# Kernel tuning notes

Measured on AMD Instinct MI355X. Metric: run time of the kernel, lower is better.

## Reference

```python
import jax, jax.numpy as jnp
import numpy as np

N_OBJECTS = 32  # mask labels 1..32 (0 = background)


def setup_inputs() -> dict:
    key = jax.random.key(0)
    k1, k2, k3, k4 = jax.random.split(key, 4)
    B, F, H, W = 8, 64, 256, 256
    encoded = jax.random.normal(k1, (B, F, H, W), dtype=jnp.float32)
    masks = jax.random.randint(k2, (B, 1, H, W), 0, N_OBJECTS + 1, dtype=jnp.int32)
    W1 = jax.random.normal(k3, (2 * F, F // 2), dtype=jnp.float32) * 0.05
    b1 = jnp.zeros((F // 2,), dtype=jnp.float32)
    W2 = jax.random.normal(k4, (F // 2, 4), dtype=jnp.float32) * 0.05
    b2 = jnp.zeros((4,), dtype=jnp.float32)
    return {"encoded": encoded, "masks": masks, "W1": W1, "b1": b1, "W2": W2, "b2": b2}


def reference(encoded, masks, W1, b1, W2, b2):
    B, F, H, W = encoded.shape
    # --- masked per-object max-pool (segment max over pixels) ---
    enc = encoded.reshape(B, F, H * W).transpose(0, 2, 1)  # [B, HW, F]
    ids = masks.reshape(B, H * W)                          # [B, HW]
    seg_max = jax.vmap(
        lambda d, i: jax.ops.segment_max(d, i, num_segments=N_OBJECTS + 1)
    )(enc, ids)                                            # [B, N+1, F]
    vectors = seg_max[:, 1:, :]                            # [B, N, F] (skip label 0)

    # --- O(N^2) pairwise MLP: connections[b,c,j,i] = sigmoid(MLP([v_i; v_j])) ---
    N = vectors.shape[1]
    vi = jnp.broadcast_to(vectors[:, :, None, :], (B, N, N, F))  # v_i over axis 1
    vj = jnp.broadcast_to(vectors[:, None, :, :], (B, N, N, F))  # v_j over axis 2
    pairs = jnp.concatenate([vi, vj], axis=-1)                   # [B, N, N, 2F]
    h = jnp.einsum('bijd,dh->bijh', pairs, W1) + b1
    out = jax.nn.sigmoid(jnp.einsum('bijh,hc->bijc', h, W2) + b2)  # [B, Ni, Nj, C]
    connections = out.transpose(0, 3, 2, 1)                        # [B, C, Nj, Ni]
    return vectors, connections
```

## Files before the change

kernel.cpp:

```cpp
#include <hip/hip_runtime.h>
#include <math.h>

#define B_      8
#define F_      64
#define HW_     65536
#define NSEG    33
#define NOBJ    32
#define FPB     8
#define SLICES  16
#define PIXB    (HW_ / SLICES)

__global__ __launch_bounds__(256) void segmax_kernel(
        const float* __restrict__ enc, const int* __restrict__ masks,
        float* __restrict__ part) {
    __shared__ float acc[FPB * NSEG * 32];
    const int tid = threadIdx.x;
    const int blk = blockIdx.x;
    const int b     = blk >> 7;
    const int fg    = (blk >> 4) & 7;
    const int slice = blk & 15;

    for (int i = tid; i < FPB * NSEG * 32; i += 256) acc[i] = -INFINITY;
    __syncthreads();

    const int fl = tid >> 5;
    const int l  = tid & 31;
    float* a = acc + fl * (NSEG * 32) + l;

    const float4* ep = (const float4*)(enc + ((size_t)(b * F_ + fg * FPB + fl)) * HW_
                                       + slice * PIXB) + l;
    const int4*   mp = (const int4*)(masks + (size_t)b * HW_ + slice * PIXB) + l;

    #pragma unroll 8
    for (int c = 0; c < PIXB / 128; ++c) {
        float4 v  = ep[c * 32];
        int4   id = mp[c * 32];
        float o;
        o = a[id.x * 32]; a[id.x * 32] = fmaxf(o, v.x);
        o = a[id.y * 32]; a[id.y * 32] = fmaxf(o, v.y);
        o = a[id.z * 32]; a[id.z * 32] = fmaxf(o, v.z);
        o = a[id.w * 32]; a[id.w * 32] = fmaxf(o, v.w);
    }
    __syncthreads();

    float* dst = part + ((size_t)(b * SLICES + slice) * NOBJ) * F_;
    {
        const int f = tid & 7, s = (tid >> 3) + 1;
        const float* row = acc + f * (NSEG * 32) + s * 32;
        float m = -INFINITY;
        #pragma unroll
        for (int k = 0; k < 32; k += 4) {
            float4 q = *(const float4*)(row + k);
            m = fmaxf(m, fmaxf(fmaxf(q.x, q.y), fmaxf(q.z, q.w)));
        }
        dst[(s - 1) * F_ + fg * FPB + f] = m;
    }
}

__global__ __launch_bounds__(256) void mlp_kernel(
        const float* __restrict__ part,
        const float* __restrict__ W1, const float* __restrict__ b1,
        const float* __restrict__ W2, const float* __restrict__ b2,
        float* __restrict__ out_vec, float* __restrict__ out_conn) {
    const int b   = blockIdx.x >> 2;
    const int it  = blockIdx.x & 3;
    const int tid = threadIdx.x;
    __shared__ float v[NOBJ * 68];
    __shared__ float w1s[2 * F_ * 32];
    __shared__ float w2s[32 * 4];
    __shared__ float b1s[32];
    __shared__ float Am[8 * 36];
    __shared__ float Bm[NOBJ * 36];

    for (int i = tid; i < 2 * F_ * 32 / 4; i += 256)
        ((float4*)w1s)[i] = ((const float4*)W1)[i];
    if (tid < 32) { w2s[tid*4+0]=W2[tid*4+0]; w2s[tid*4+1]=W2[tid*4+1];
                    w2s[tid*4+2]=W2[tid*4+2]; w2s[tid*4+3]=W2[tid*4+3];
                    b1s[tid] = b1[tid]; }

    const float4* p4 = (const float4*)(part + (size_t)b * SLICES * NOBJ * F_);
    for (int cell = tid; cell < NOBJ * 16; cell += 256) {
        const int s = cell >> 4, f4 = cell & 15;
        float4 m = {-INFINITY, -INFINITY, -INFINITY, -INFINITY};
        #pragma unroll
        for (int sl = 0; sl < SLICES; ++sl) {
            float4 q = p4[((size_t)sl * NOBJ + s) * (F_ / 4) + f4];
            m.x = fmaxf(m.x, q.x); m.y = fmaxf(m.y, q.y);
            m.z = fmaxf(m.z, q.z); m.w = fmaxf(m.w, q.w);
        }
        *(float4*)(v + s * 68 + f4 * 4) = m;
        if (it == 0) ((float4*)(out_vec + (size_t)b * NOBJ * F_))[cell] = m;
    }
    __syncthreads();

    for (int d = tid; d < 320; d += 256) {
        int kg, obj, half;
        if (d < 64) { half = 0; obj = it * 8 + (d >> 3); kg = d & 7; }
        else        { half = 1; obj = (d - 64) >> 3;     kg = d & 7; }
        const float* vv = v + obj * 68;
        const float* w  = w1s + half * (F_ * 32) + kg * 4;
        float4 s4 = {0.f, 0.f, 0.f, 0.f};
        #pragma unroll
        for (int f = 0; f < F_; ++f) {
            float4 wf = *(const float4*)(w + f * 32);
            float x = vv[f];
            s4.x = fmaf(x, wf.x, s4.x); s4.y = fmaf(x, wf.y, s4.y);
            s4.z = fmaf(x, wf.z, s4.z); s4.w = fmaf(x, wf.w, s4.w);
        }
        if (half == 0) {
            float4 bb = *(const float4*)(b1s + kg * 4);
            s4.x += bb.x; s4.y += bb.y; s4.z += bb.z; s4.w += bb.w;
            *(float4*)(Am + (d >> 3) * 36 + kg * 4) = s4;
        } else {
            *(float4*)(Bm + obj * 36 + kg * 4) = s4;
        }
    }
    __syncthreads();

    {
        int i_loc = tid >> 5, j = tid & 31;
        float o0 = b2[0], o1 = b2[1], o2 = b2[2], o3 = b2[3];
        #pragma unroll
        for (int kg = 0; kg < 8; ++kg) {
            float4 ha = *(const float4*)(Am + i_loc * 36 + kg * 4);
            float4 hb = *(const float4*)(Bm + j * 36 + kg * 4);
            float h0 = ha.x + hb.x, h1 = ha.y + hb.y;
            float h2 = ha.z + hb.z, h3 = ha.w + hb.w;
            const float* w2 = w2s + kg * 16;
            o0 = fmaf(h0, w2[0],  fmaf(h1, w2[4],  fmaf(h2, w2[8],  fmaf(h3, w2[12], o0))));
            o1 = fmaf(h0, w2[1],  fmaf(h1, w2[5],  fmaf(h2, w2[9],  fmaf(h3, w2[13], o1))));
            o2 = fmaf(h0, w2[2],  fmaf(h1, w2[6],  fmaf(h2, w2[10], fmaf(h3, w2[14], o2))));
            o3 = fmaf(h0, w2[3],  fmaf(h1, w2[7],  fmaf(h2, w2[11], fmaf(h3, w2[15], o3))));
        }
        float* oc = out_conn + (size_t)b * 4 * NOBJ * NOBJ + j * NOBJ + (it * 8 + i_loc);
        oc[0 * NOBJ * NOBJ] = 1.f / (1.f + expf(-o0));
        oc[1 * NOBJ * NOBJ] = 1.f / (1.f + expf(-o1));
        oc[2 * NOBJ * NOBJ] = 1.f / (1.f + expf(-o2));
        oc[3 * NOBJ * NOBJ] = 1.f / (1.f + expf(-o3));
    }
}

extern "C" void kernel_launch(void* const* d_in, const int* in_sizes, int n_in,
                              void* d_out, int out_size, void* d_ws, size_t ws_size,
                              hipStream_t stream) {
    const float* enc   = (const float*)d_in[0];
    const int*   masks = (const int*)  d_in[1];
    const float* W1    = (const float*)d_in[2];
    const float* b1    = (const float*)d_in[3];
    const float* W2    = (const float*)d_in[4];
    const float* b2    = (const float*)d_in[5];

    float* out_vec  = (float*)d_out;
    float* out_conn = out_vec + B_ * NOBJ * F_;
    float* part     = (float*)d_ws;

    segmax_kernel<<<B_ * (F_ / FPB) * SLICES, 256, 0, stream>>>(enc, masks, part);
    mlp_kernel<<<B_ * 4, 256, 0, stream>>>(part, W1, b1, W2, b2, out_vec, out_conn);
}
```

Measured before the change: 210.1 us.

## Fuse segment-max and pairwise MLP via last-block-done atomic counter

```diff
diff --git a/kernel.cpp b/kernel.cpp
--- a/kernel.cpp
+++ b/kernel.cpp
@@ -9,17 +9,35 @@
 #define FPB     8
 #define SLICES  16
 #define PIXB    (HW_ / SLICES)
+#define BLOCKS_PER_B ((F_ / FPB) * SLICES)
 
-__global__ __launch_bounds__(256) void segmax_kernel(
+union SharedU {
+    float acc[FPB * NSEG * 32];
+    struct {
+        float v[NOBJ * 68];
+        float w1s[2 * F_ * 32];
+        float w2s[NOBJ * 4];
+        float b1s[NOBJ];
+        float Cm[NOBJ * 36];
+        float Bm[NOBJ * 36];
+    } m;
+};
+
+__global__ __launch_bounds__(256) void fused_kernel(
         const float* __restrict__ enc, const int* __restrict__ masks,
-        float* __restrict__ part) {
-    __shared__ float acc[FPB * NSEG * 32];
+        const float* __restrict__ W1, const float* __restrict__ b1,
+        const float* __restrict__ W2, const float* __restrict__ b2,
+        float* __restrict__ part, int* __restrict__ cnt,
+        float* __restrict__ out_vec, float* __restrict__ out_conn) {
+    __shared__ SharedU sh;
+    __shared__ int is_last;
     const int tid = threadIdx.x;
     const int blk = blockIdx.x;
     const int b     = blk >> 7;
     const int fg    = (blk >> 4) & 7;
     const int slice = blk & 15;
 
+    float* acc = sh.acc;
     for (int i = tid; i < FPB * NSEG * 32; i += 256) acc[i] = -INFINITY;
     __syncthreads();
 
@@ -43,8 +61,8 @@
     }
     __syncthreads();
 
-    float* dst = part + ((size_t)(b * SLICES + slice) * NOBJ) * F_;
     {
+        float* dst = part + ((size_t)(b * SLICES + slice) * NOBJ) * F_;
         const int f = tid & 7, s = (tid >> 3) + 1;
         const float* row = acc + f * (NSEG * 32) + s * 32;
         float m = -INFINITY;
@@ -55,22 +73,23 @@
         }
         dst[(s - 1) * F_ + fg * FPB + f] = m;
     }
-}
 
-__global__ __launch_bounds__(256) void mlp_kernel(
-        const float* __restrict__ part,
-        const float* __restrict__ W1, const float* __restrict__ b1,
-        const float* __restrict__ W2, const float* __restrict__ b2,
-        float* __restrict__ out_vec, float* __restrict__ out_conn) {
-    const int b   = blockIdx.x >> 2;
-    const int it  = blockIdx.x & 3;
-    const int tid = threadIdx.x;
-    __shared__ float v[NOBJ * 68];
-    __shared__ float w1s[2 * F_ * 32];
-    __shared__ float w2s[32 * 4];
-    __shared__ float b1s[32];
-    __shared__ float Am[8 * 36];
-    __shared__ float Bm[NOBJ * 36];
+    __syncthreads();
+    if (tid == 0) {
+        __threadfence();
+        int t = atomicAdd(&cnt[b], 1);
+        is_last = (t == BLOCKS_PER_B - 1);
+    }
+    __syncthreads();
+    if (!is_last) return;
+    __threadfence();
+
+    float* v   = sh.m.v;
+    float* w1s = sh.m.w1s;
+    float* w2s = sh.m.w2s;
+    float* b1s = sh.m.b1s;
+    float* Cm  = sh.m.Cm;
+    float* Bm  = sh.m.Bm;
 
     for (int i = tid; i < 2 * F_ * 32 / 4; i += 256)
         ((float4*)w1s)[i] = ((const float4*)W1)[i];
@@ -89,14 +108,14 @@
             m.z = fmaxf(m.z, q.z); m.w = fmaxf(m.w, q.w);
         }
         *(float4*)(v + s * 68 + f4 * 4) = m;
-        if (it == 0) ((float4*)(out_vec + (size_t)b * NOBJ * F_))[cell] = m;
+        ((float4*)(out_vec + (size_t)b * NOBJ * F_))[cell] = m;
     }
     __syncthreads();
 
-    for (int d = tid; d < 320; d += 256) {
-        int kg, obj, half;
-        if (d < 64) { half = 0; obj = it * 8 + (d >> 3); kg = d & 7; }
-        else        { half = 1; obj = (d - 64) >> 3;     kg = d & 7; }
+    for (int d = tid; d < 512; d += 256) {
+        const int half = d >> 8;
+        const int obj  = (d >> 3) & 31;
+        const int kg   = d & 7;
         const float* vv = v + obj * 68;
         const float* w  = w1s + half * (F_ * 32) + kg * 4;
         float4 s4 = {0.f, 0.f, 0.f, 0.f};
@@ -110,7 +129,7 @@
         if (half == 0) {
             float4 bb = *(const float4*)(b1s + kg * 4);
             s4.x += bb.x; s4.y += bb.y; s4.z += bb.z; s4.w += bb.w;
-            *(float4*)(Am + (d >> 3) * 36 + kg * 4) = s4;
+            *(float4*)(Cm + obj * 36 + kg * 4) = s4;
         } else {
             *(float4*)(Bm + obj * 36 + kg * 4) = s4;
         }
@@ -118,25 +137,31 @@
     __syncthreads();
 
     {
-        int i_loc = tid >> 5, j = tid & 31;
-        float o0 = b2[0], o1 = b2[1], o2 = b2[2], o3 = b2[3];
+        const int j  = tid & 31;
+        const int i0 = tid >> 5;
+        const float bb0 = b2[0], bb1 = b2[1], bb2 = b2[2], bb3 = b2[3];
         #pragma unroll
-        for (int kg = 0; kg < 8; ++kg) {
-            float4 ha = *(const float4*)(Am + i_loc * 36 + kg * 4);
-            float4 hb = *(const float4*)(Bm + j * 36 + kg * 4);
-            float h0 = ha.x + hb.x, h1 = ha.y + hb.y;
-            float h2 = ha.z + hb.z, h3 = ha.w + hb.w;
-            const float* w2 = w2s + kg * 16;
-            o0 = fmaf(h0, w2[0],  fmaf(h1, w2[4],  fmaf(h2, w2[8],  fmaf(h3, w2[12], o0))));
-            o1 = fmaf(h0, w2[1],  fmaf(h1, w2[5],  fmaf(h2, w2[9],  fmaf(h3, w2[13], o1))));
-            o2 = fmaf(h0, w2[2],  fmaf(h1, w2[6],  fmaf(h2, w2[10], fmaf(h3, w2[14], o2))));
-            o3 = fmaf(h0, w2[3],  fmaf(h1, w2[7],  fmaf(h2, w2[11], fmaf(h3, w2[15], o3))));
+        for (int k = 0; k < 4; ++k) {
+            const int i = i0 + k * 8;
+            float o0 = bb0, o1 = bb1, o2 = bb2, o3 = bb3;
+            #pragma unroll
+            for (int kg = 0; kg < 8; ++kg) {
+                float4 ha = *(const float4*)(Cm + i * 36 + kg * 4);
+                float4 hb = *(const float4*)(Bm + j * 36 + kg * 4);
+                float h0 = ha.x + hb.x, h1 = ha.y + hb.y;
+                float h2 = ha.z + hb.z, h3 = ha.w + hb.w;
+                const float* w2 = w2s + kg * 16;
+                o0 = fmaf(h0, w2[0],  fmaf(h1, w2[4],  fmaf(h2, w2[8],  fmaf(h3, w2[12], o0))));
+                o1 = fmaf(h0, w2[1],  fmaf(h1, w2[5],  fmaf(h2, w2[9],  fmaf(h3, w2[13], o1))));
+                o2 = fmaf(h0, w2[2],  fmaf(h1, w2[6],  fmaf(h2, w2[10], fmaf(h3, w2[14], o2))));
+                o3 = fmaf(h0, w2[3],  fmaf(h1, w2[7],  fmaf(h2, w2[11], fmaf(h3, w2[15], o3))));
+            }
+            float* oc = out_conn + (size_t)b * 4 * NOBJ * NOBJ + j * NOBJ + i;
+            oc[0 * NOBJ * NOBJ] = 1.f / (1.f + expf(-o0));
+            oc[1 * NOBJ * NOBJ] = 1.f / (1.f + expf(-o1));
+            oc[2 * NOBJ * NOBJ] = 1.f / (1.f + expf(-o2));
+            oc[3 * NOBJ * NOBJ] = 1.f / (1.f + expf(-o3));
         }
-        float* oc = out_conn + (size_t)b * 4 * NOBJ * NOBJ + j * NOBJ + (it * 8 + i_loc);
-        oc[0 * NOBJ * NOBJ] = 1.f / (1.f + expf(-o0));
-        oc[1 * NOBJ * NOBJ] = 1.f / (1.f + expf(-o1));
-        oc[2 * NOBJ * NOBJ] = 1.f / (1.f + expf(-o2));
-        oc[3 * NOBJ * NOBJ] = 1.f / (1.f + expf(-o3));
     }
 }
 
@@ -153,7 +178,9 @@
     float* out_vec  = (float*)d_out;
     float* out_conn = out_vec + B_ * NOBJ * F_;
     float* part     = (float*)d_ws;
+    int*   cnt      = (int*)((char*)d_ws + (size_t)B_ * SLICES * NOBJ * F_ * 4);
 
-    segmax_kernel<<<B_ * (F_ / FPB) * SLICES, 256, 0, stream>>>(enc, masks, part);
-    mlp_kernel<<<B_ * 4, 256, 0, stream>>>(part, W1, b1, W2, b2, out_vec, out_conn);
+    hipMemsetAsync(cnt, 0, B_ * sizeof(int), stream);
+    fused_kernel<<<B_ * BLOCKS_PER_B, 256, 0, stream>>>(
+        enc, masks, W1, b1, W2, b2, part, cnt, out_vec, out_conn);
 }
```

After: 269.8 us. +28.4%, slower.
